# Kernel tuning notes

Measured on AMD Instinct MI355X. Metric: run time of the kernel, lower is better.

## Reference

```python
import jax, jax.numpy as jnp
import numpy as np

B, IC, HW = 16, 32, 128
NF, OC, K, GROUP = 8, 64, 5, 8


def _rotate_filters(w, theta):
    """Bilinear rotation of filters w [N, C, k, k] by angle theta.
    Matches torch affine_grid + grid_sample (align_corners=False, zero padding)."""
    k = w.shape[-1]
    base = (2.0 * jnp.arange(k, dtype=w.dtype) + 1.0) / k - 1.0  # pixel-center normalized coords
    ys, xs = jnp.meshgrid(base, base, indexing='ij')  # [k, k]
    c, s = jnp.cos(theta), jnp.sin(theta)
    # sampling grid = rot_mat @ [x, y, 1]
    gx = c * xs - s * ys
    gy = s * xs + c * ys
    # normalized -> pixel coords (align_corners=False)
    ix = ((gx + 1.0) * k - 1.0) / 2.0
    iy = ((gy + 1.0) * k - 1.0) / 2.0
    x0 = jnp.floor(ix)
    y0 = jnp.floor(iy)
    wx1 = ix - x0
    wy1 = iy - y0
    wx0 = 1.0 - wx1
    wy0 = 1.0 - wy1

    def gather(yy, xx):
        valid = ((xx >= 0) & (xx < k) & (yy >= 0) & (yy < k)).astype(w.dtype)
        xc = jnp.clip(xx, 0, k - 1).astype(jnp.int32)
        yc = jnp.clip(yy, 0, k - 1).astype(jnp.int32)
        return w[:, :, yc, xc] * valid  # [N, C, k, k]

    return (gather(y0, x0) * (wy0 * wx0)
            + gather(y0, x0 + 1.0) * (wy0 * wx1)
            + gather(y0 + 1.0, x0) * (wy1 * wx0)
            + gather(y0 + 1.0, x0 + 1.0) * (wy1 * wx1))


def _forward(x, kernel, relaxed_weights):
    nf, oc, ic, k, _ = kernel.shape
    group = relaxed_weights.shape[1]
    wflat = kernel.reshape(nf * oc, ic, k, k)
    thetas = -2.0 * jnp.pi / group * jnp.arange(group, dtype=x.dtype)
    # [group, nf*oc, ic, k, k]
    fb = jax.vmap(lambda t: _rotate_filters(wflat, t))(thetas)
    # -> [nf, oc, group, ic, k, k]
    fb = jnp.transpose(fb, (1, 0, 2, 3, 4)).reshape(nf, oc, group, ic, k, k)
    w = jnp.einsum('na,noaikl->oaikl', relaxed_weights, fb)
    w = w.reshape(oc * group, ic, k, k)
    pad = (k - 1) // 2
    y = jax.lax.conv_general_dilated(
        x, w, window_strides=(1, 1), padding=[(pad, pad), (pad, pad)],
        dimension_numbers=('NCHW', 'OIHW', 'NCHW'))
    b, _, h, wd = y.shape
    y = y.reshape(b, oc, group, wd, h)  # matches torch .view(B, O, A, W, H)
    return jax.nn.leaky_relu(y, negative_slope=0.01)


def setup_inputs() -> dict:
    key = jax.random.key(0)
    k1, k2, k3 = jax.random.split(key, 3)
    x = jax.random.normal(k1, (B, IC, HW, HW), dtype=jnp.float32)
    kernel = jax.random.normal(k2, (NF, OC, IC, K, K), dtype=jnp.float32) * 0.05
    relaxed_weights = jax.random.normal(k3, (NF, GROUP), dtype=jnp.float32)
    return {"x": x, "kernel": kernel, "relaxed_weights": relaxed_weights}


def reference(x, kernel, relaxed_weights):
    return _forward(x, kernel, relaxed_weights)
```

## Files before the change

kernel.cpp:

```cpp
#include <hip/hip_runtime.h>
#include <hip/hip_bf16.h>
#include <math.h>

#define B_   16
#define IC_  32
#define HW_  128
#define NF_  8
#define OC_  64
#define K_   5
#define GRP_ 8
#define COTOT_ (OC_ * GRP_)
#define XTH  132
#define TAPSTRIDE (COTOT_ * IC_)
#define XROWB (XTH * IC_ * 2)

typedef short  short8  __attribute__((ext_vector_type(8)));
typedef unsigned short ushort8 __attribute__((ext_vector_type(8)));
typedef float  f32x4   __attribute__((ext_vector_type(4)));

static __device__ inline unsigned short f2bf(float f) {
    unsigned u = __builtin_bit_cast(unsigned, f);
    unsigned r = (u + 0x7FFFu + ((u >> 16) & 1u)) >> 16;
    return (unsigned short)r;
}

__device__ __forceinline__ void gload16(void* lds, const void* g) {
    __builtin_amdgcn_global_load_lds(
        (const __attribute__((address_space(1))) unsigned int*)g,
        (__attribute__((address_space(3))) unsigned int*)lds, 16, 0, 0);
}

__global__ __launch_bounds__(256) void xform_kernel(
    const float* __restrict__ x, unsigned short* __restrict__ xt) {
    int idx = blockIdx.x * blockDim.x + threadIdx.x;
    const int TOT = B_ * XTH * XTH;
    if (idx >= TOT) return;
    int wp = idx % XTH;
    int t  = idx / XTH;
    int hp = t % XTH;
    int b  = t / XTH;

    unsigned short vals[IC_];
    bool interior = (hp >= 2) && (hp < 2 + HW_) && (wp >= 2) && (wp < 2 + HW_);
    if (interior) {
        const float* xb = x + ((size_t)b * IC_) * (HW_ * HW_) + (hp - 2) * HW_ + (wp - 2);
        #pragma unroll
        for (int ic = 0; ic < IC_; ++ic)
            vals[ic] = f2bf(xb[(size_t)ic * (HW_ * HW_)]);
    } else {
        #pragma unroll
        for (int ic = 0; ic < IC_; ++ic) vals[ic] = 0;
    }
    ushort8* dst = (ushort8*)(xt + (size_t)idx * IC_);
    #pragma unroll
    for (int c = 0; c < 4; ++c) {
        ushort8 v;
        #pragma unroll
        for (int j = 0; j < 8; ++j) v[j] = vals[c * 8 + j];
        dst[c] = v;
    }
}

__global__ __launch_bounds__(256) void build_w_kernel(
    const float* __restrict__ kern,
    const float* __restrict__ relaxed,
    unsigned short* __restrict__ wt) {
    int idx = blockIdx.x * blockDim.x + threadIdx.x;
    const int TOT = 25 * COTOT_ * IC_;
    if (idx >= TOT) return;
    int ic = idx & (IC_ - 1);
    int t  = idx >> 5;
    int co = t & (COTOT_ - 1);
    int e  = t >> 9;
    int a  = co & (GRP_ - 1);
    int o  = co >> 3;
    int i  = e / K_;
    int j  = e - i * K_;

    float theta = -6.283185307179586f / (float)GRP_ * (float)a;
    float cth = cosf(theta), sth = sinf(theta);
    float bx = (2.0f * (float)j + 1.0f) / (float)K_ - 1.0f;
    float by = (2.0f * (float)i + 1.0f) / (float)K_ - 1.0f;
    float gx = cth * bx - sth * by;
    float gy = sth * bx + cth * by;
    float ix = ((gx + 1.0f) * (float)K_ - 1.0f) * 0.5f;
    float iy = ((gy + 1.0f) * (float)K_ - 1.0f) * 0.5f;
    float x0 = floorf(ix), y0 = floorf(iy);
    float wx1 = ix - x0, wy1 = iy - y0;
    float wx0 = 1.0f - wx1, wy0 = 1.0f - wy1;

    float xs2[2]  = {x0, x0 + 1.0f};
    float ys2[2]  = {y0, y0 + 1.0f};
    float wxs[2] = {wx0, wx1};
    float wys[2] = {wy0, wy1};

    float tw[4];
    int   tyc[4], txc[4];
    #pragma unroll
    for (int dy = 0; dy < 2; ++dy) {
        #pragma unroll
        for (int dx = 0; dx < 2; ++dx) {
            float xx = xs2[dx], yy = ys2[dy];
            bool valid = (xx >= 0.0f) && (xx < (float)K_) &&
                         (yy >= 0.0f) && (yy < (float)K_);
            int tp = dy * 2 + dx;
            tw[tp]  = wys[dy] * wxs[dx] * (valid ? 1.0f : 0.0f);
            txc[tp] = (int)fminf(fmaxf(xx, 0.0f), (float)(K_ - 1));
            tyc[tp] = (int)fminf(fmaxf(yy, 0.0f), (float)(K_ - 1));
        }
    }

    float acc = 0.0f;
    #pragma unroll
    for (int n = 0; n < NF_; ++n) {
        const float* kb = kern + ((size_t)((n * OC_ + o) * IC_ + ic)) * (K_ * K_);
        float v = 0.0f;
        #pragma unroll
        for (int tp = 0; tp < 4; ++tp)
            v += kb[tyc[tp] * K_ + txc[tp]] * tw[tp];
        acc += relaxed[n * GRP_ + a] * v;
    }
    wt[idx] = f2bf(acc);
}

#define PREF_AF(dst, tap) {                                                   \
    const unsigned short* wp_ = wl + (size_t)(tap) * TAPSTRIDE;               \
    _Pragma("unroll")                                                         \
    for (int m = 0; m < 8; ++m)                                               \
        dst[m] = *(const short8*)(wp_ + (size_t)m * 16 * IC_);                \
}

#define PREF_BF(dst) {                                                        \
    int base_ = prow + (pkx + l15) * 64 +                                     \
                ((l4 ^ (((pkx + l15) & 7) >> 1)) << 4);                       \
    _Pragma("unroll")                                                         \
    for (int n = 0; n < 8; ++n)                                               \
        dst[n] = *(const short8*)(xsb + base_ + n * 1024);                    \
    if (++pkx == 5) { pkx = 0; prow += XROWB; }                               \
}

#define COMP(afx, bfx) {                                                      \
    __builtin_amdgcn_s_setprio(1);                                            \
    _Pragma("unroll")                                                         \
    for (int m = 0; m < 8; ++m)                                               \
        _Pragma("unroll")                                                     \
        for (int n = 0; n < 8; ++n)                                           \
            acc[m][n] = __builtin_amdgcn_mfma_f32_16x16x32_bf16(              \
                afx[m], bfx[n], acc[m][n], 0, 0, 0);                          \
    __builtin_amdgcn_s_setprio(0);                                            \
}

__global__ __launch_bounds__(256, 1) void conv_mfma_kernel(
    const unsigned short* __restrict__ xt,
    const unsigned short* __restrict__ wt,
    float* __restrict__ out) {
    __shared__ __align__(16) unsigned short xs[8 * XTH * IC_];

    int tid  = threadIdx.x;
    int lane = tid & 63;
    int wv   = tid >> 6;
    int l15  = lane & 15;
    int l4   = lane >> 4;

    int hp = blockIdx.x;
    int b  = blockIdx.y;
    int cg = blockIdx.z;
    int cobase = cg * 128;
    int h0 = hp * 4;

    {
        const unsigned short* xb = xt + (((size_t)b * XTH + h0) * XTH) * IC_;
        #pragma unroll
        for (int i = 0; i < 17; ++i) {
            int s = i * 256 + tid;
            if (s < 4224) {
                int row = s / 528;
                int rem = s - row * 528;
                int w   = rem >> 2;
                int p   = rem & 3;
                int c   = p ^ ((w >> 1) & 3);
                gload16(&xs[s * 8], xb + row * (XTH * IC_) + w * 32 + c * 8);
            }
        }
    }

    const unsigned short* wl = wt + (size_t)(cobase + l15) * IC_ + l4 * 8;

    short8 afA[8], afB[8];
    PREF_AF(afA, 0);

    f32x4 acc[8][8];
    #pragma unroll
    for (int m = 0; m < 8; ++m)
        #pragma unroll
        for (int n = 0; n < 8; ++n) acc[m][n] = (f32x4)(0.0f);

    __syncthreads();

    const char* xsb = (const char*)xs;
    int pkx  = 0;
    int prow = wv * XROWB;

    short8 bfA[8], bfB[8];
    PREF_BF(bfA);

    #pragma unroll 1
    for (int pi = 0; pi < 12; ++pi) {
        int t0 = pi * 2;
        PREF_AF(afB, t0 + 1);
        PREF_BF(bfB);
        COMP(afA, bfA);
        PREF_AF(afA, t0 + 2);
        PREF_BF(bfA);
        COMP(afB, bfB);
    }
    COMP(afA, bfA);

    int h = h0 + wv;
    float* ob = out + ((size_t)b * COTOT_ + cobase) * (HW_ * HW_)
                    + (size_t)h * HW_;
    #pragma unroll
    for (int m = 0; m < 8; ++m) {
        #pragma unroll
        for (int n = 0; n < 8; ++n) {
            #pragma unroll
            for (int r = 0; r < 4; ++r) {
                int co = m * 16 + l4 * 4 + r;
                int w  = n * 16 + l15;
                float v = acc[m][n][r];
                v = (v >= 0.0f) ? v : 0.01f * v;
                ob[(size_t)co * (HW_ * HW_) + w] = v;
            }
        }
    }
}

extern "C" void kernel_launch(void* const* d_in, const int* in_sizes, int n_in,
                              void* d_out, int out_size, void* d_ws, size_t ws_size,
                              hipStream_t stream) {
    const float* x       = (const float*)d_in[0];
    const float* kernel  = (const float*)d_in[1];
    const float* relaxed = (const float*)d_in[2];
    float* out = (float*)d_out;

    unsigned short* xt = (unsigned short*)d_ws;
    unsigned short* wt = (unsigned short*)((char*)d_ws + (size_t)B_ * XTH * XTH * IC_ * 2);

    const int xtot = B_ * XTH * XTH;
    xform_kernel<<<(xtot + 255) / 256, 256, 0, stream>>>(x, xt);

    const int wtot = 25 * COTOT_ * IC_;
    build_w_kernel<<<(wtot + 255) / 256, 256, 0, stream>>>(kernel, relaxed, wt);

    dim3 grid(HW_ / 4, B_, COTOT_ / 128);
    conv_mfma_kernel<<<grid, 256, 0, stream>>>(xt, wt, out);
}
```

Measured before the change: 257.7 us.

## Switch conv to 32x32x16 MFMA and process two row strips per block

Result: slower. 307.1 us (+19.2%).

```diff
diff --git a/kernel.cpp b/kernel.cpp
--- a/kernel.cpp
+++ b/kernel.cpp
@@ -13,10 +13,11 @@
 #define XTH  132
 #define TAPSTRIDE (COTOT_ * IC_)
 #define XROWB (XTH * IC_ * 2)
+#define HW2  (HW_ * HW_)
 
 typedef short  short8  __attribute__((ext_vector_type(8)));
 typedef unsigned short ushort8 __attribute__((ext_vector_type(8)));
-typedef float  f32x4   __attribute__((ext_vector_type(4)));
+typedef float  f32x16  __attribute__((ext_vector_type(16)));
 
 static __device__ inline unsigned short f2bf(float f) {
     unsigned u = __builtin_bit_cast(unsigned, f);
@@ -43,10 +44,10 @@
     unsigned short vals[IC_];
     bool interior = (hp >= 2) && (hp < 2 + HW_) && (wp >= 2) && (wp < 2 + HW_);
     if (interior) {
-        const float* xb = x + ((size_t)b * IC_) * (HW_ * HW_) + (hp - 2) * HW_ + (wp - 2);
+        const float* xb = x + ((size_t)b * IC_) * HW2 + (hp - 2) * HW_ + (wp - 2);
         #pragma unroll
         for (int ic = 0; ic < IC_; ++ic)
-            vals[ic] = f2bf(xb[(size_t)ic * (HW_ * HW_)]);
+            vals[ic] = f2bf(xb[(size_t)ic * HW2]);
     } else {
         #pragma unroll
         for (int ic = 0; ic < IC_; ++ic) vals[ic] = 0;
@@ -126,27 +127,35 @@
 #define PREF_AF(dst, tap) {                                                   \
     const unsigned short* wp_ = wl + (size_t)(tap) * TAPSTRIDE;               \
     _Pragma("unroll")                                                         \
-    for (int m = 0; m < 8; ++m)                                               \
-        dst[m] = *(const short8*)(wp_ + (size_t)m * 16 * IC_);                \
+    for (int mf = 0; mf < 4; ++mf)                                            \
+        _Pragma("unroll")                                                     \
+        for (int kk = 0; kk < 2; ++kk)                                        \
+            dst[mf * 2 + kk] = *(const short8*)(wp_ + mf * 1024 + kk * 16);   \
 }
 
 #define PREF_BF(dst) {                                                        \
-    int base_ = prow + (pkx + l15) * 64 +                                     \
-                ((l4 ^ (((pkx + l15) & 7) >> 1)) << 4);                       \
+    int sw_ = ((pkx + l31) >> 1) & 3;                                         \
+    int wb_ = prow + (pkx + l31) * 64;                                        \
     _Pragma("unroll")                                                         \
-    for (int n = 0; n < 8; ++n)                                               \
-        dst[n] = *(const short8*)(xsb + base_ + n * 1024);                    \
+    for (int nf = 0; nf < 4; ++nf)                                            \
+        _Pragma("unroll")                                                     \
+        for (int kk = 0; kk < 2; ++kk) {                                      \
+            int p_ = (kk * 2 + lhi) ^ sw_;                                    \
+            dst[nf * 2 + kk] = *(const short8*)(xsb + wb_ + nf * 2048 + p_ * 16); \
+        }                                                                     \
     if (++pkx == 5) { pkx = 0; prow += XROWB; }                               \
 }
 
 #define COMP(afx, bfx) {                                                      \
     __builtin_amdgcn_s_setprio(1);                                            \
     _Pragma("unroll")                                                         \
-    for (int m = 0; m < 8; ++m)                                               \
+    for (int mf = 0; mf < 4; ++mf)                                            \
         _Pragma("unroll")                                                     \
-        for (int n = 0; n < 8; ++n)                                           \
-            acc[m][n] = __builtin_amdgcn_mfma_f32_16x16x32_bf16(              \
-                afx[m], bfx[n], acc[m][n], 0, 0, 0);                          \
+        for (int nf = 0; nf < 4; ++nf)                                        \
+            _Pragma("unroll")                                                 \
+            for (int kk = 0; kk < 2; ++kk)                                    \
+                acc[mf][nf] = __builtin_amdgcn_mfma_f32_32x32x16_bf16(        \
+                    afx[mf * 2 + kk], bfx[nf * 2 + kk], acc[mf][nf], 0, 0, 0);\
     __builtin_amdgcn_s_setprio(0);                                            \
 }
 
@@ -159,77 +168,84 @@
     int tid  = threadIdx.x;
     int lane = tid & 63;
     int wv   = tid >> 6;
-    int l15  = lane & 15;
-    int l4   = lane >> 4;
+    int l31  = lane & 31;
+    int lhi  = lane >> 5;
 
     int hp = blockIdx.x;
     int b  = blockIdx.y;
     int cg = blockIdx.z;
     int cobase = cg * 128;
-    int h0 = hp * 4;
-
-    {
-        const unsigned short* xb = xt + (((size_t)b * XTH + h0) * XTH) * IC_;
-        #pragma unroll
-        for (int i = 0; i < 17; ++i) {
-            int s = i * 256 + tid;
-            if (s < 4224) {
-                int row = s / 528;
-                int rem = s - row * 528;
-                int w   = rem >> 2;
-                int p   = rem & 3;
-                int c   = p ^ ((w >> 1) & 3);
-                gload16(&xs[s * 8], xb + row * (XTH * IC_) + w * 32 + c * 8);
+
+    const unsigned short* wl = wt + (size_t)(cobase + l31) * IC_ + lhi * 8;
+    const char* xsb = (const char*)xs;
+
+    #pragma unroll 1
+    for (int s = 0; s < 2; ++s) {
+        int h0 = hp * 8 + s * 4;
+
+        if (s) __syncthreads();
+
+        {
+            const unsigned short* xb = xt + (((size_t)b * XTH + h0) * XTH) * IC_;
+            #pragma unroll
+            for (int i = 0; i < 17; ++i) {
+                int sl = i * 256 + tid;
+                if (sl < 4224) {
+                    int row = sl / 528;
+                    int rem = sl - row * 528;
+                    int w   = rem >> 2;
+                    int p   = rem & 3;
+                    int c   = p ^ ((w >> 1) & 3);
+                    gload16(&xs[sl * 8], xb + row * (XTH * IC_) + w * 32 + c * 8);
+                }
             }
         }
-    }
-
-    const unsigned short* wl = wt + (size_t)(cobase + l15) * IC_ + l4 * 8;
-
-    short8 afA[8], afB[8];
-    PREF_AF(afA, 0);
-
-    f32x4 acc[8][8];
-    #pragma unroll
-    for (int m = 0; m < 8; ++m)
-        #pragma unroll
-        for (int n = 0; n < 8; ++n) acc[m][n] = (f32x4)(0.0f);
-
-    __syncthreads();
-
-    const char* xsb = (const char*)xs;
-    int pkx  = 0;
-    int prow = wv * XROWB;
-
-    short8 bfA[8], bfB[8];
-    PREF_BF(bfA);
-
-    #pragma unroll 1
-    for (int pi = 0; pi < 12; ++pi) {
-        int t0 = pi * 2;
-        PREF_AF(afB, t0 + 1);
-        PREF_BF(bfB);
+
+        short8 afA[8], afB[8];
+        PREF_AF(afA, 0);
+
+        f32x16 acc[4][4];
+        #pragma unroll
+        for (int mf = 0; mf < 4; ++mf)
+            #pragma unroll
+            for (int nf = 0; nf < 4; ++nf) acc[mf][nf] = (f32x16)(0.0f);
+
+        __syncthreads();
+
+        int pkx  = 0;
+        int prow = wv * XROWB;
+
+        short8 bfA[8], bfB[8];
+        PREF_BF(bfA);
+
+        #pragma unroll 1
+        for (int pi = 0; pi < 12; ++pi) {
+            int t0 = pi * 2;
+            PREF_AF(afB, t0 + 1);
+            PREF_BF(bfB);
+            COMP(afA, bfA);
+            PREF_AF(afA, t0 + 2);
+            PREF_BF(bfA);
+            COMP(afB, bfB);
+        }
         COMP(afA, bfA);
-        PREF_AF(afA, t0 + 2);
-        PREF_BF(bfA);
-        COMP(afB, bfB);
-    }
-    COMP(afA, bfA);
-
-    int h = h0 + wv;
-    float* ob = out + ((size_t)b * COTOT_ + cobase) * (HW_ * HW_)
-                    + (size_t)h * HW_;
-    #pragma unroll
-    for (int m = 0; m < 8; ++m) {
-        #pragma unroll
-        for (int n = 0; n < 8; ++n) {
+
+        __builtin_amdgcn_s_barrier();
+
+        int h = h0 + wv;
+        float* ob = out + ((size_t)b * COTOT_ + cobase) * HW2 + (size_t)h * HW_;
+        #pragma unroll
+        for (int mf = 0; mf < 4; ++mf) {
             #pragma unroll
-            for (int r = 0; r < 4; ++r) {
-                int co = m * 16 + l4 * 4 + r;
-                int w  = n * 16 + l15;
-                float v = acc[m][n][r];
-                v = (v >= 0.0f) ? v : 0.01f * v;
-                ob[(size_t)co * (HW_ * HW_) + w] = v;
+            for (int nf = 0; nf < 4; ++nf) {
+                #pragma unroll
+                for (int r = 0; r < 16; ++r) {
+                    int co = mf * 32 + (r & 3) + 8 * (r >> 2) + 4 * lhi;
+                    int w  = nf * 32 + l31;
+                    float v = acc[mf][nf][r];
+                    v = (v >= 0.0f) ? v : 0.01f * v;
+                    ob[(size_t)co * HW2 + w] = v;
+                }
             }
         }
     }
@@ -252,6 +268,6 @@
     const int wtot = 25 * COTOT_ * IC_;
     build_w_kernel<<<(wtot + 255) / 256, 256, 0, stream>>>(kernel, relaxed, wt);
 
-    dim3 grid(HW_ / 4, B_, COTOT_ / 128);
+    dim3 grid(HW_ / 8, B_, COTOT_ / 128);
     conv_mfma_kernel<<<grid, 256, 0, stream>>>(xt, wt, out);
 }
```

## Replace LDS-staged conv tile with persistent blocks reading input directly from global

Applied to the files above, without the earlier changes.

Measured after the change: 759.6 us. 195% more time.

```diff
diff --git a/kernel.cpp b/kernel.cpp
--- a/kernel.cpp
+++ b/kernel.cpp
@@ -12,7 +12,7 @@
 #define COTOT_ (OC_ * GRP_)
 #define XTH  132
 #define TAPSTRIDE (COTOT_ * IC_)
-#define XROWB (XTH * IC_ * 2)
+#define HW2  (HW_ * HW_)
 
 typedef short  short8  __attribute__((ext_vector_type(8)));
 typedef unsigned short ushort8 __attribute__((ext_vector_type(8)));
@@ -22,12 +22,6 @@
     unsigned u = __builtin_bit_cast(unsigned, f);
     unsigned r = (u + 0x7FFFu + ((u >> 16) & 1u)) >> 16;
     return (unsigned short)r;
-}
-
-__device__ __forceinline__ void gload16(void* lds, const void* g) {
-    __builtin_amdgcn_global_load_lds(
-        (const __attribute__((address_space(1))) unsigned int*)g,
-        (__attribute__((address_space(3))) unsigned int*)lds, 16, 0, 0);
 }
 
 __global__ __launch_bounds__(256) void xform_kernel(
@@ -43,10 +37,10 @@
     unsigned short vals[IC_];
     bool interior = (hp >= 2) && (hp < 2 + HW_) && (wp >= 2) && (wp < 2 + HW_);
     if (interior) {
-        const float* xb = x + ((size_t)b * IC_) * (HW_ * HW_) + (hp - 2) * HW_ + (wp - 2);
+        const float* xb = x + ((size_t)b * IC_) * HW2 + (hp - 2) * HW_ + (wp - 2);
         #pragma unroll
         for (int ic = 0; ic < IC_; ++ic)
-            vals[ic] = f2bf(xb[(size_t)ic * (HW_ * HW_)]);
+            vals[ic] = f2bf(xb[(size_t)ic * HW2]);
     } else {
         #pragma unroll
         for (int ic = 0; ic < IC_; ++ic) vals[ic] = 0;
@@ -131,12 +125,10 @@
 }
 
 #define PREF_BF(dst) {                                                        \
-    int base_ = prow + (pkx + l15) * 64 +                                     \
-                ((l4 ^ (((pkx + l15) & 7) >> 1)) << 4);                       \
     _Pragma("unroll")                                                         \
-    for (int n = 0; n < 8; ++n)                                               \
-        dst[n] = *(const short8*)(xsb + base_ + n * 1024);                    \
-    if (++pkx == 5) { pkx = 0; prow += XROWB; }                               \
+    for (int n = 0; n < 4; ++n)                                               \
+        dst[n] = *(const short8*)(xbl + poff + n * 512);                      \
+    if (++pkx == 5) { pkx = 0; poff += (XTH - 4) * 32; } else poff += 32;     \
 }
 
 #define COMP(afx, bfx) {                                                      \
@@ -144,92 +136,78 @@
     _Pragma("unroll")                                                         \
     for (int m = 0; m < 8; ++m)                                               \
         _Pragma("unroll")                                                     \
-        for (int n = 0; n < 8; ++n)                                           \
+        for (int n = 0; n < 4; ++n)                                           \
             acc[m][n] = __builtin_amdgcn_mfma_f32_16x16x32_bf16(              \
                 afx[m], bfx[n], acc[m][n], 0, 0, 0);                          \
     __builtin_amdgcn_s_setprio(0);                                            \
 }
 
-__global__ __launch_bounds__(256, 1) void conv_mfma_kernel(
+__global__ __launch_bounds__(256, 2) void conv_mfma_kernel(
     const unsigned short* __restrict__ xt,
     const unsigned short* __restrict__ wt,
     float* __restrict__ out) {
-    __shared__ __align__(16) unsigned short xs[8 * XTH * IC_];
-
     int tid  = threadIdx.x;
     int lane = tid & 63;
     int wv   = tid >> 6;
     int l15  = lane & 15;
     int l4   = lane >> 4;
-
-    int hp = blockIdx.x;
-    int b  = blockIdx.y;
-    int cg = blockIdx.z;
-    int cobase = cg * 128;
-    int h0 = hp * 4;
-
-    {
-        const unsigned short* xb = xt + (((size_t)b * XTH + h0) * XTH) * IC_;
-        #pragma unroll
-        for (int i = 0; i < 17; ++i) {
-            int s = i * 256 + tid;
-            if (s < 4224) {
-                int row = s / 528;
-                int rem = s - row * 528;
-                int w   = rem >> 2;
-                int p   = rem & 3;
-                int c   = p ^ ((w >> 1) & 3);
-                gload16(&xs[s * 8], xb + row * (XTH * IC_) + w * 32 + c * 8);
-            }
+    int hr   = wv >> 1;
+    int wn   = wv & 1;
+
+    int bid = blockIdx.x;
+
+    #pragma unroll 1
+    for (int i = 0; i < 8; ++i) {
+        int unit = bid + (i << 9);
+        int cg = unit >> 10;
+        int b  = (unit >> 6) & 15;
+        int hp = unit & 63;
+        int h0 = hp * 2;
+        int cobase = cg * 128;
+
+        const unsigned short* wl = wt + (size_t)(cobase + l15) * IC_ + l4 * 8;
+        const unsigned short* xbl = xt +
+            ((size_t)(b * XTH + h0 + hr) * XTH + wn * 64 + l15) * IC_ + l4 * 8;
+
+        short8 afA[8], afB[8], bfA[4], bfB[4];
+        int pkx = 0, poff = 0;
+
+        PREF_AF(afA, 0);
+        PREF_BF(bfA);
+
+        f32x4 acc[8][4];
+        #pragma unroll
+        for (int m = 0; m < 8; ++m)
+            #pragma unroll
+            for (int n = 0; n < 4; ++n) acc[m][n] = (f32x4)(0.0f);
+
+        #pragma unroll 1
+        for (int pi = 0; pi < 12; ++pi) {
+            int t0 = pi * 2;
+            PREF_AF(afB, t0 + 1);
+            PREF_BF(bfB);
+            COMP(afA, bfA);
+            PREF_AF(afA, t0 + 2);
+            PREF_BF(bfA);
+            COMP(afB, bfB);
         }
-    }
-
-    const unsigned short* wl = wt + (size_t)(cobase + l15) * IC_ + l4 * 8;
-
-    short8 afA[8], afB[8];
-    PREF_AF(afA, 0);
-
-    f32x4 acc[8][8];
-    #pragma unroll
-    for (int m = 0; m < 8; ++m)
-        #pragma unroll
-        for (int n = 0; n < 8; ++n) acc[m][n] = (f32x4)(0.0f);
-
-    __syncthreads();
-
-    const char* xsb = (const char*)xs;
-    int pkx  = 0;
-    int prow = wv * XROWB;
-
-    short8 bfA[8], bfB[8];
-    PREF_BF(bfA);
-
-    #pragma unroll 1
-    for (int pi = 0; pi < 12; ++pi) {
-        int t0 = pi * 2;
-        PREF_AF(afB, t0 + 1);
-        PREF_BF(bfB);
         COMP(afA, bfA);
-        PREF_AF(afA, t0 + 2);
-        PREF_BF(bfA);
-        COMP(afB, bfB);
-    }
-    COMP(afA, bfA);
-
-    int h = h0 + wv;
-    float* ob = out + ((size_t)b * COTOT_ + cobase) * (HW_ * HW_)
-                    + (size_t)h * HW_;
-    #pragma unroll
-    for (int m = 0; m < 8; ++m) {
-        #pragma unroll
-        for (int n = 0; n < 8; ++n) {
+
+        int h = h0 + hr;
+        float* ob = out + ((size_t)b * COTOT_ + cobase) * HW2
+                        + (size_t)h * HW_ + wn * 64;
+        #pragma unroll
+        for (int m = 0; m < 8; ++m) {
             #pragma unroll
-            for (int r = 0; r < 4; ++r) {
-                int co = m * 16 + l4 * 4 + r;
-                int w  = n * 16 + l15;
-                float v = acc[m][n][r];
-                v = (v >= 0.0f) ? v : 0.01f * v;
-                ob[(size_t)co * (HW_ * HW_) + w] = v;
+            for (int n = 0; n < 4; ++n) {
+                #pragma unroll
+                for (int r = 0; r < 4; ++r) {
+                    int co = m * 16 + l4 * 4 + r;
+                    int w  = n * 16 + l15;
+                    float v = acc[m][n][r];
+                    v = fmaxf(v, 0.01f * v);
+                    ob[(size_t)co * HW2 + w] = v;
+                }
             }
         }
     }
@@ -252,6 +230,5 @@
     const int wtot = 25 * COTOT_ * IC_;
     build_w_kernel<<<(wtot + 255) / 256, 256, 0, stream>>>(kernel, relaxed, wt);
 
-    dim3 grid(HW_ / 4, B_, COTOT_ / 128);
-    conv_mfma_kernel<<<grid, 256, 0, stream>>>(xt, wt, out);
-}
+    conv_mfma_kernel<<<512, 256, 0, stream>>>(xt, wt, out);
+}
```
